# Kernel optimization log

Hardware: AMD Instinct MI355X
Metric: run time of the kernel (lower is better)

The kernel has to match this reference:

```python
import jax, jax.numpy as jnp
import numpy as np

E = 32      # feature/query dim
H = 4       # heads
HD = E // H # head dim = 8
N_LAYERS = 12
N_Q = 16
B = 128
S = 512


def _mha(q, kv, Wqkv, bqkv, Wo, bo):
    # PyTorch nn.MultiheadAttention (batch_first), eval mode (no dropout).
    Wq, Wk, Wv = jnp.split(Wqkv, 3, axis=0)   # each [E, E]
    bq, bk, bv = jnp.split(bqkv, 3)

    def heads(x, W, b):
        y = x @ W.T + b                         # [B, L, E]
        b_, l_, _ = y.shape
        return y.reshape(b_, l_, H, HD).transpose(0, 2, 1, 3)  # [B, H, L, HD]

    qh, kh, vh = heads(q, Wq, bq), heads(kv, Wk, bk), heads(kv, Wv, bv)
    scores = jnp.einsum('bhqd,bhkd->bhqk', qh, kh) / np.sqrt(HD).astype(np.float32)
    att = jax.nn.softmax(scores, axis=-1)
    o = jnp.einsum('bhqk,bhkd->bhqd', att, vh)
    o = o.transpose(0, 2, 1, 3).reshape(q.shape[0], q.shape[1], E)
    return o @ Wo.T + bo


def setup_inputs() -> dict:
    key = jax.random.key(0)
    ks = iter(jax.random.split(key, 64))
    g = lambda shape, s=0.05: (jax.random.normal(next(ks), shape, dtype=jnp.float32) * s)
    inp = {
        'x_omic': jax.random.normal(next(ks), (B, 80), dtype=jnp.float32),
        'x_path': jax.random.normal(next(ks), (B, S, E), dtype=jnp.float32),
        # frozen omic FFN encoder: 80 -> 64 -> 48 -> 32 -> 32, ELU each
        'omic_W0': g((64, 80)), 'omic_b0': g((64,)),
        'omic_W1': g((48, 64)), 'omic_b1': g((48,)),
        'omic_W2': g((32, 48)), 'omic_b2': g((32,)),
        'omic_W3': g((E, 32)),  'omic_b3': g((E,)),
        'ln_g': jnp.ones((E,), jnp.float32), 'ln_b': jnp.zeros((E,), jnp.float32),
        'corr_Wqkv': g((3 * E, E)), 'corr_bqkv': g((3 * E,)),
        'corr_Wo': g((E, E)), 'corr_bo': g((E,)),
        # 12 stacked query<->omic and query<->path cross-attentions
        'qo_Wqkv': g((N_LAYERS, 3 * E, E)), 'qo_bqkv': g((N_LAYERS, 3 * E)),
        'qo_Wo': g((N_LAYERS, E, E)), 'qo_bo': g((N_LAYERS, E)),
        'qp_Wqkv': g((N_LAYERS, 3 * E, E)), 'qp_bqkv': g((N_LAYERS, 3 * E)),
        'qp_Wo': g((N_LAYERS, E, E)), 'qp_bo': g((N_LAYERS, E)),
        # 12 stacked 2-layer FFNs (Linear-ReLU-Linear, no residual in source)
        'ffn_W1': g((N_LAYERS, E, E)), 'ffn_b1': g((N_LAYERS, E)),
        'ffn_W2': g((N_LAYERS, E, E)), 'ffn_b2': g((N_LAYERS, E)),
        'Qs': jax.random.normal(next(ks), (N_Q, E), dtype=jnp.float32),
        'grade_W': g((3, E)), 'grade_b': g((3,)),
        'haz_W': g((1, E)), 'haz_b': g((1,)),
    }
    return inp


def reference(x_omic, x_path, omic_W0, omic_b0, omic_W1, omic_b1, omic_W2, omic_b2,
              omic_W3, omic_b3, ln_g, ln_b, corr_Wqkv, corr_bqkv, corr_Wo, corr_bo,
              qo_Wqkv, qo_bqkv, qo_Wo, qo_bo, qp_Wqkv, qp_bqkv, qp_Wo, qp_bo,
              ffn_W1, ffn_b1, ffn_W2, ffn_b2, Qs, grade_W, grade_b, haz_W, haz_b):
    # frozen omic encoder (eval mode: AlphaDropout is identity)
    h = jax.nn.elu(x_omic @ omic_W0.T + omic_b0)
    h = jax.nn.elu(h @ omic_W1.T + omic_b1)
    h = jax.nn.elu(h @ omic_W2.T + omic_b2)
    omic_emb = jax.nn.elu(h @ omic_W3.T + omic_b3)[:, None, :]   # [B, 1, E]

    qs = jnp.broadcast_to(Qs[None], (x_omic.shape[0], N_Q, E))    # [B, 16, E]

    # correlation self-attention on LayerNorm(x_path), residual on raw x_path
    mu = jnp.mean(x_path, axis=-1, keepdims=True)
    var = jnp.var(x_path, axis=-1, keepdims=True)
    xn = (x_path - mu) / jnp.sqrt(var + 1e-5) * ln_g + ln_b
    img = x_path + _mha(xn, xn, corr_Wqkv, corr_bqkv, corr_Wo, corr_bo)

    for i in range(N_LAYERS):
        qs = _mha(qs, omic_emb, qo_Wqkv[i], qo_bqkv[i], qo_Wo[i], qo_bo[i])
        qs = _mha(qs, img, qp_Wqkv[i], qp_bqkv[i], qp_Wo[i], qp_bo[i])
        qs = jax.nn.relu(qs @ ffn_W1[i].T + ffn_b1[i]) @ ffn_W2[i].T + ffn_b2[i]

    features = qs.mean(axis=1)                                    # [B, E]
    grade = jax.nn.log_softmax(features @ grade_W.T + grade_b, axis=1)
    hazard = jax.nn.sigmoid(features @ haz_W.T + haz_b) * 6.0 - 3.0
    return features, grade, hazard
```

## Files before the change

kernel.cpp:

```cpp
#include <hip/hip_runtime.h>
#include <hip/hip_bf16.h>

typedef __attribute__((ext_vector_type(8))) short short8;
typedef __attribute__((ext_vector_type(4))) float f32x4;

__device__ __forceinline__ float elu1(float x) { return x > 0.f ? x : expm1f(x); }
__device__ __forceinline__ unsigned pkbf(float a, float b) {
  return (unsigned)__bfloat16_as_ushort(__float2bfloat16(a)) |
         ((unsigned)__bfloat16_as_ushort(__float2bfloat16(b)) << 16);
}
__device__ __forceinline__ unsigned pk_trunc(float a, float b) {
  return (__float_as_uint(a) >> 16) | (__float_as_uint(b) & 0xffff0000u);
}
__device__ __forceinline__ short8 cvt8(float4 a, float4 b, float s) {
  uint4 u = { pkbf(a.x * s, a.y * s), pkbf(a.z * s, a.w * s),
              pkbf(b.x * s, b.y * s), pkbf(b.z * s, b.w * s) };
  union { uint4 u4; short8 s8; } c; c.u4 = u; return c.s8;
}

__global__ __launch_bounds__(512, 4) void k_fattn(
    const float* __restrict__ xp, const float* __restrict__ ln_g, const float* __restrict__ ln_b,
    const float* __restrict__ Wqkv, const float* __restrict__ bqkv,
    ushort* __restrict__ obf)
{
  __shared__ ushort qlds[512 * 8];
  __shared__ ushort klds[512 * 8];
  __shared__ ushort vts[8 * 512];
  __shared__ ushort ps[8][2][16 * 64];

  const float sc = 0.35355339059327373f * 1.4426950408889634f;
  int tid = threadIdx.x, w = tid >> 6, lane = tid & 63;
  int g = lane >> 4, qr = lane & 15;
  int bh = blockIdx.x, b = bh >> 2, h = bh & 3;
  const short8 z8 = {0, 0, 0, 0, 0, 0, 0, 0};

  int wrow = (qr < 8) ? (h * 8 + qr) : (32 + h * 8 + qr - 8);
  float qsc = (qr < 8) ? sc : 1.f;
  const float4* wr = (const float4*)(Wqkv + wrow * 32 + g * 8);
  short8 wqk = cvt8(wr[0], wr[1], qsc);
  short8 wv = z8;
  if (qr < 8) {
    const float4* vr = (const float4*)(Wqkv + (64 + h * 8 + qr) * 32 + g * 8);
    wv = cvt8(vr[0], vr[1], 1.f);
  }
  f32x4 bqk, bv;
  #pragma unroll
  for (int r = 0; r < 4; ++r) {
    bqk[r] = (g < 2) ? bqkv[h * 8 + g * 4 + r] * sc : bqkv[32 + h * 8 + (g - 2) * 4 + r];
    bv[r]  = (g < 2) ? bqkv[64 + h * 8 + g * 4 + r] : 0.f;
  }
  const float4* lg4 = (const float4*)(ln_g + g * 8);
  const float4* lb4 = (const float4*)(ln_b + g * 8);
  float4 ga = lg4[0], gb2 = lg4[1], ba = lb4[0], bb2 = lb4[1];

  #pragma unroll
  for (int i = 0; i < 4; ++i) {
    int rloc = w * 64 + i * 16 + qr;
    const float4* xr = (const float4*)(xp + (b * 512 + rloc) * 32 + g * 8);
    float4 x0 = xr[0], x1 = xr[1];
    float s1 = x0.x + x0.y + x0.z + x0.w + x1.x + x1.y + x1.z + x1.w;
    float s2 = x0.x*x0.x + x0.y*x0.y + x0.z*x0.z + x0.w*x0.w
             + x1.x*x1.x + x1.y*x1.y + x1.z*x1.z + x1.w*x1.w;
    s1 += __shfl_xor(s1, 16); s1 += __shfl_xor(s1, 32);
    s2 += __shfl_xor(s2, 16); s2 += __shfl_xor(s2, 32);
    float mu = s1 * 0.03125f;
    float rs = rsqrtf(s2 * 0.03125f - mu * mu + 1e-5f);
    float4 n0 = { (x0.x-mu)*rs*ga.x+ba.x, (x0.y-mu)*rs*ga.y+ba.y,
                  (x0.z-mu)*rs*ga.z+ba.z, (x0.w-mu)*rs*ga.w+ba.w };
    float4 n1 = { (x1.x-mu)*rs*gb2.x+bb2.x, (x1.y-mu)*rs*gb2.y+bb2.y,
                  (x1.z-mu)*rs*gb2.z+bb2.z, (x1.w-mu)*rs*gb2.w+bb2.w };
    short8 bx = cvt8(n0, n1, 1.f);

    f32x4 cqk = __builtin_amdgcn_mfma_f32_16x16x32_bf16(wqk, bx, bqk, 0, 0, 0);
    f32x4 cv  = __builtin_amdgcn_mfma_f32_16x16x32_bf16(wv,  bx, bv,  0, 0, 0);
    uint2 o2 = { pkbf(cqk[0], cqk[1]), pkbf(cqk[2], cqk[3]) };
    ushort* dst = (g < 2) ? qlds : klds;
    *(uint2*)(dst + rloc * 8 + (g & 1) * 4) = o2;
    if (g < 2) {
      #pragma unroll
      for (int r = 0; r < 4; ++r)
        vts[(g * 4 + r) * 512 + rloc] = __bfloat16_as_ushort(__float2bfloat16(cv[r]));
    }
  }
  __syncthreads();

  const short8 one8 = {(short)0x3F80, (short)0x3F80, (short)0x3F80, (short)0x3F80,
                       (short)0x3F80, (short)0x3F80, (short)0x3F80, (short)0x3F80};
  unsigned swz = (unsigned)(qr & 7) << 4;
  char* p0 = (char*)&ps[w][0][0] + qr * 128;
  char* p1 = (char*)&ps[w][1][0] + qr * 128;

  #pragma unroll
  for (int p = 0; p < 2; ++p) {
    int qbase = w * 64 + p * 32;
    short8 qf0 = (g == 0) ? *(const short8*)(qlds + (qbase + qr) * 8) : z8;
    short8 qf1 = (g == 0) ? *(const short8*)(qlds + (qbase + 16 + qr) * 8) : z8;
    f32x4 ot0 = {0.f, 0.f, 0.f, 0.f}, ot1 = {0.f, 0.f, 0.f, 0.f};

    for (int c = 0; c < 8; ++c) {
      const short8* vp = (const short8*)(vts + qr * 512 + c * 64 + g * 8);
      short8 vf0 = (qr < 8) ? vp[0] : (qr == 8 ? one8 : z8);
      short8 vf1 = (qr < 8) ? vp[4] : (qr == 8 ? one8 : z8);
      #pragma unroll
      for (int t = 0; t < 4; ++t) {
        short8 af = (g == 0) ? *(const short8*)(klds + (c * 64 + t * 16 + qr) * 8) : z8;
        f32x4 sa = __builtin_amdgcn_mfma_f32_16x16x32_bf16(af, qf0, (f32x4){0.f,0.f,0.f,0.f}, 0, 0, 0);
        f32x4 sb = __builtin_amdgcn_mfma_f32_16x16x32_bf16(af, qf1, (f32x4){0.f,0.f,0.f,0.f}, 0, 0, 0);
        unsigned off = (unsigned)((t * 16 + g * 4) << 1) ^ swz;
        uint2 pa = { pk_trunc(__builtin_amdgcn_exp2f(sa[0]), __builtin_amdgcn_exp2f(sa[1])),
                     pk_trunc(__builtin_amdgcn_exp2f(sa[2]), __builtin_amdgcn_exp2f(sa[3])) };
        uint2 pb2 = { pk_trunc(__builtin_amdgcn_exp2f(sb[0]), __builtin_amdgcn_exp2f(sb[1])),
                      pk_trunc(__builtin_amdgcn_exp2f(sb[2]), __builtin_amdgcn_exp2f(sb[3])) };
        *(uint2*)(p0 + off) = pa;
        *(uint2*)(p1 + off) = pb2;
      }
      #pragma unroll
      for (int tp = 0; tp < 2; ++tp) {
        unsigned off = (unsigned)((tp * 32 + g * 8) << 1) ^ swz;
        short8 vv = tp ? vf1 : vf0;
        short8 pba = *(const short8*)(p0 + off);
        short8 pbb = *(const short8*)(p1 + off);
        ot0 = __builtin_amdgcn_mfma_f32_16x16x32_bf16(vv, pba, ot0, 0, 0, 0);
        ot1 = __builtin_amdgcn_mfma_f32_16x16x32_bf16(vv, pbb, ot1, 0, 0, 0);
      }
    }
    #pragma unroll
    for (int qg = 0; qg < 2; ++qg) {
      f32x4 ot = qg ? ot1 : ot0;
      float lpv = __shfl(ot[0], 32 + qr, 64);
      float rl = 1.f / lpv;
      if (g < 2) {
        int rowg = bh * 512 + qbase + qg * 16 + qr;
        uint2 o2 = { pkbf(ot[0] * rl, ot[1] * rl), pkbf(ot[2] * rl, ot[3] * rl) };
        *(uint2*)((unsigned*)obf + rowg * 4 + g * 2) = o2;
      }
    }
  }
}

__global__ __launch_bounds__(256) void k_final(
    const ushort* __restrict__ obf, const float* __restrict__ xp,
    const float* __restrict__ Wo, const float* __restrict__ bo,
    const float* __restrict__ xo,
    const float* __restrict__ oW0, const float* __restrict__ ob0,
    const float* __restrict__ oW1, const float* __restrict__ ob1,
    const float* __restrict__ oW2, const float* __restrict__ ob2,
    const float* __restrict__ oW3, const float* __restrict__ ob3,
    const float* __restrict__ qoW, const float* __restrict__ qob,
    const float* __restrict__ qoWo, const float* __restrict__ qobo,
    const float* __restrict__ qpW, const float* __restrict__ qpb,
    const float* __restrict__ qpWo, const float* __restrict__ qpbo,
    const float* __restrict__ fW1, const float* __restrict__ fb1,
    const float* __restrict__ fW2, const float* __restrict__ fb2,
    const float* __restrict__ gW, const float* __restrict__ gb,
    const float* __restrict__ hW, const float* __restrict__ hb,
    float* __restrict__ out)
{
  __shared__ float4 imgl[512 * 8];
  __shared__ float p[4][512];
  __shared__ float partial[8][4][32];
  __shared__ float buf1[80], buf2[64];
  __shared__ float emb[32], qbar[32], qh[32], u[4][32], cc4[4], lsum[4], ctx4[4][32], t32[32], o32[32];
  int b = blockIdx.x, tid = threadIdx.x;
  int w = tid >> 6, lane = tid & 63, g = lane >> 4, qr = lane & 15;

  {
    short8 wa[2]; f32x4 bc2[2];
    #pragma unroll
    for (int t = 0; t < 2; ++t) {
      const float4* wrr = (const float4*)(Wo + (t * 16 + qr) * 32 + g * 8);
      wa[t] = cvt8(wrr[0], wrr[1], 1.f);
      const float4 bb = *(const float4*)(bo + t * 16 + g * 4);
      bc2[t] = (f32x4){bb.x, bb.y, bb.z, bb.w};
    }
    #pragma unroll
    for (int j = 0; j < 8; ++j) {
      int rloc = j * 64 + w * 16 + qr;
      short8 ob = *(const short8*)(obf + ((b * 4 + g) * 512 + rloc) * 8);
      #pragma unroll
      for (int t = 0; t < 2; ++t) {
        f32x4 ct = __builtin_amdgcn_mfma_f32_16x16x32_bf16(wa[t], ob, bc2[t], 0, 0, 0);
        int e4 = t * 4 + g;
        float4 xv = *(const float4*)(xp + (b * 512 + rloc) * 32 + e4 * 4);
        imgl[rloc * 8 + (e4 ^ (rloc & 7))] =
            (float4){ xv.x + ct[0], xv.y + ct[1], xv.z + ct[2], xv.w + ct[3] };
      }
    }
  }
  __syncthreads();

  if (tid < 80) buf1[tid] = xo[b * 80 + tid];
  __syncthreads();
  if (tid < 64) { float a = ob0[tid]; const float* wgt = oW0 + tid * 80;
    for (int e = 0; e < 80; ++e) a += buf1[e] * wgt[e]; buf2[tid] = elu1(a); }
  __syncthreads();
  if (tid < 48) { float a = ob1[tid]; const float* wgt = oW1 + tid * 64;
    for (int e = 0; e < 64; ++e) a += buf2[e] * wgt[e]; buf1[tid] = elu1(a); }
  __syncthreads();
  if (tid < 32) { float a = ob2[tid]; const float* wgt = oW2 + tid * 48;
    for (int e = 0; e < 48; ++e) a += buf1[e] * wgt[e]; buf2[tid] = elu1(a); }
  __syncthreads();
  if (tid < 32) { float a = ob3[tid]; const float* wgt = oW3 + tid * 32;
    for (int e = 0; e < 32; ++e) a += buf2[e] * wgt[e]; emb[tid] = elu1(a); }
  __syncthreads();

  if (tid < 32) { float a = qob[64 + tid]; const float* wgt = qoW + (64 + tid) * 32;
    for (int e = 0; e < 32; ++e) a += emb[e] * wgt[e]; t32[tid] = a; }
  __syncthreads();
  if (tid < 32) { float a = qobo[tid]; const float* wgt = qoWo + tid * 32;
    for (int e = 0; e < 32; ++e) a += t32[e] * wgt[e]; qbar[tid] = a; }
  __syncthreads();

  if (tid < 32) { float a = qpb[tid]; const float* wgt = qpW + tid * 32;
    for (int e = 0; e < 32; ++e) a += qbar[e] * wgt[e]; qh[tid] = a; }
  __syncthreads();
  if (tid < 128) {
    int hh = tid >> 5, e = tid & 31;
    float a = 0.f;
    #pragma unroll
    for (int d = 0; d < 8; ++d) a += qh[hh * 8 + d] * qpW[(32 + hh * 8 + d) * 32 + e];
    u[hh][e] = a;
    if (e == 0) { float c2 = 0.f; for (int d = 0; d < 8; ++d) c2 += qh[hh * 8 + d] * qpb[32 + hh * 8 + d]; cc4[hh] = c2; }
  }
  __syncthreads();

  #pragma unroll
  for (int j = 0; j < 8; ++j) {
    int idx = tid + j * 256; int hh = idx >> 9, kk = idx & 511;
    const float* uh = u[hh];
    float a = cc4[hh];
    #pragma unroll
    for (int e4 = 0; e4 < 8; ++e4) {
      float4 t = imgl[kk * 8 + (e4 ^ (kk & 7))];
      a += uh[e4 * 4] * t.x + uh[e4 * 4 + 1] * t.y + uh[e4 * 4 + 2] * t.z + uh[e4 * 4 + 3] * t.w;
    }
    p[hh][kk] = __builtin_amdgcn_exp2f(fminf(a * 0.51006979f, 115.f));
  }
  __syncthreads();
  {
    int ww = tid >> 6, ln2 = tid & 63;
    float a = 0.f;
    for (int kk = ln2; kk < 512; kk += 64) a += p[ww][kk];
    #pragma unroll
    for (int m = 32; m >= 1; m >>= 1) a += __shfl_xor(a, m, 64);
    if (ln2 == 0) lsum[ww] = 1.f / a;
  }
  {
    int e = tid & 31, ch = tid >> 5;
    float a0 = 0.f, a1 = 0.f, a2 = 0.f, a3 = 0.f;
    for (int kk = ch * 64; kk < ch * 64 + 64; ++kk) {
      float val = ((const float*)&imgl[kk * 8 + ((e >> 2) ^ (kk & 7))])[e & 3];
      a0 += p[0][kk] * val; a1 += p[1][kk] * val; a2 += p[2][kk] * val; a3 += p[3][kk] * val;
    }
    partial[ch][0][e] = a0; partial[ch][1][e] = a1; partial[ch][2][e] = a2; partial[ch][3][e] = a3;
  }
  __syncthreads();
  if (tid < 128) {
    int hh = tid >> 5, e = tid & 31;
    float a = 0.f;
    #pragma unroll
    for (int ch = 0; ch < 8; ++ch) a += partial[ch][hh][e];
    ctx4[hh][e] = a * lsum[hh];
  }
  __syncthreads();
  if (tid < 32) { int hh = tid >> 3;
    float a = qpb[64 + tid]; const float* wgt = qpW + (64 + tid) * 32;
    for (int e = 0; e < 32; ++e) a += ctx4[hh][e] * wgt[e]; o32[tid] = a; }
  __syncthreads();
  if (tid < 32) { float a = qpbo[tid]; const float* wgt = qpWo + tid * 32;
    for (int e = 0; e < 32; ++e) a += o32[e] * wgt[e]; t32[tid] = a; }
  __syncthreads();

  if (tid < 32) { float a = fb1[tid]; const float* wgt = fW1 + tid * 32;
    for (int e = 0; e < 32; ++e) a += t32[e] * wgt[e]; o32[tid] = fmaxf(a, 0.f); }
  __syncthreads();
  if (tid < 32) { float a = fb2[tid]; const float* wgt = fW2 + tid * 32;
    for (int e = 0; e < 32; ++e) a += o32[e] * wgt[e]; qbar[tid] = a; }
  __syncthreads();

  if (tid < 32) out[b * 32 + tid] = qbar[tid];
  if (tid == 0) {
    float g0 = gb[0], g1 = gb[1], g2 = gb[2];
    for (int e = 0; e < 32; ++e) { float f = qbar[e]; g0 += f * gW[e]; g1 += f * gW[32 + e]; g2 += f * gW[64 + e]; }
    float m = fmaxf(g0, fmaxf(g1, g2));
    float lse = m + logf(expf(g0 - m) + expf(g1 - m) + expf(g2 - m));
    float* og = out + 4096;
    og[b * 3 + 0] = g0 - lse; og[b * 3 + 1] = g1 - lse; og[b * 3 + 2] = g2 - lse;
    float hz = hb[0];
    for (int e = 0; e < 32; ++e) hz += qbar[e] * hW[e];
    out[4480 + b] = 1.f / (1.f + expf(-hz)) * 6.f - 3.f;
  }
}

extern "C" void kernel_launch(void* const* d_in, const int* in_sizes, int n_in,
                              void* d_out, int out_size, void* d_ws, size_t ws_size,
                              hipStream_t stream) {
  const float* x_omic = (const float*)d_in[0];
  const float* x_path = (const float*)d_in[1];
  const float* oW0 = (const float*)d_in[2];  const float* ob0 = (const float*)d_in[3];
  const float* oW1 = (const float*)d_in[4];  const float* ob1 = (const float*)d_in[5];
  const float* oW2 = (const float*)d_in[6];  const float* ob2 = (const float*)d_in[7];
  const float* oW3 = (const float*)d_in[8];  const float* ob3 = (const float*)d_in[9];
  const float* ln_g = (const float*)d_in[10]; const float* ln_b = (const float*)d_in[11];
  const float* cW  = (const float*)d_in[12]; const float* cb  = (const float*)d_in[13];
  const float* cWo = (const float*)d_in[14]; const float* cbo = (const float*)d_in[15];
  const float* qoW = (const float*)d_in[16]; const float* qob = (const float*)d_in[17];
  const float* qoWo = (const float*)d_in[18]; const float* qobo = (const float*)d_in[19];
  const float* qpW = (const float*)d_in[20]; const float* qpb = (const float*)d_in[21];
  const float* qpWo = (const float*)d_in[22]; const float* qpbo = (const float*)d_in[23];
  const float* fW1 = (const float*)d_in[24]; const float* fb1 = (const float*)d_in[25];
  const float* fW2 = (const float*)d_in[26]; const float* fb2 = (const float*)d_in[27];
  const float* gW = (const float*)d_in[29]; const float* gb = (const float*)d_in[30];
  const float* hW = (const float*)d_in[31]; const float* hb = (const float*)d_in[32];

  float* out = (float*)d_out;
  ushort* obf = (ushort*)d_ws;

  const int L = 11;
  k_fattn<<<512, 512, 0, stream>>>(x_path, ln_g, ln_b, cW, cb, obf);
  k_final<<<128, 256, 0, stream>>>(obf, x_path, cWo, cbo, x_omic,
      oW0, ob0, oW1, ob1, oW2, ob2, oW3, ob3,
      qoW + L * 96 * 32, qob + L * 96, qoWo + L * 32 * 32, qobo + L * 32,
      qpW + L * 96 * 32, qpb + L * 96, qpWo + L * 32 * 32, qpbo + L * 32,
      fW1 + L * 32 * 32, fb1 + L * 32, fW2 + L * 32 * 32, fb2 + L * 32,
      gW, gb, hW, hb, out);
}
```

Measured before the change: 53.78 us.

## Restructure flash attention into one pass over four query tiles; widen final kernel

The attention kernel now loads all four 16-row Q fragments of a wave at once. It streams each K/V chunk a single time, running QK, exp and PV for every Q tile through one reused per-wave P buffer. This halves the LDS used for P and removes the redundant second pass over K/V. Packing exp values to bf16 now uses a single byte-permute instead of shift and mask. The K-operand masking and the zero V rows are dropped because they do not affect the output rows that are written. Separately, the final kernel doubles its block to 512 threads, splitting the image projection, score and context loops across more waves with more partial sums. The cost is higher register pressure from four accumulators and four Q fragments per wave.

```diff
diff --git a/kernel.cpp b/kernel.cpp
--- a/kernel.cpp
+++ b/kernel.cpp
@@ -9,13 +9,13 @@
   return (unsigned)__bfloat16_as_ushort(__float2bfloat16(a)) |
          ((unsigned)__bfloat16_as_ushort(__float2bfloat16(b)) << 16);
 }
-__device__ __forceinline__ unsigned pk_trunc(float a, float b) {
-  return (__float_as_uint(a) >> 16) | (__float_as_uint(b) & 0xffff0000u);
-}
 __device__ __forceinline__ short8 cvt8(float4 a, float4 b, float s) {
   uint4 u = { pkbf(a.x * s, a.y * s), pkbf(a.z * s, a.w * s),
               pkbf(b.x * s, b.y * s), pkbf(b.z * s, b.w * s) };
   union { uint4 u4; short8 s8; } c; c.u4 = u; return c.s8;
+}
+__device__ __forceinline__ unsigned pk_perm(float a, float b) {
+  return __builtin_amdgcn_perm(__float_as_uint(b), __float_as_uint(a), 0x07060302u);
 }
 
 __global__ __launch_bounds__(512, 4) void k_fattn(
@@ -26,7 +26,7 @@
   __shared__ ushort qlds[512 * 8];
   __shared__ ushort klds[512 * 8];
   __shared__ ushort vts[8 * 512];
-  __shared__ ushort ps[8][2][16 * 64];
+  __shared__ ushort ps[8][16 * 64];
 
   const float sc = 0.35355339059327373f * 1.4426950408889634f;
   int tid = threadIdx.x, w = tid >> 6, lane = tid & 63;
@@ -87,58 +87,63 @@
   const short8 one8 = {(short)0x3F80, (short)0x3F80, (short)0x3F80, (short)0x3F80,
                        (short)0x3F80, (short)0x3F80, (short)0x3F80, (short)0x3F80};
   unsigned swz = (unsigned)(qr & 7) << 4;
-  char* p0 = (char*)&ps[w][0][0] + qr * 128;
-  char* p1 = (char*)&ps[w][1][0] + qr * 128;
+  char* pw = (char*)&ps[w][0] + qr * 128;
+
+  int qbase = w * 64;
+  short8 qf0 = (g == 0) ? *(const short8*)(qlds + (qbase + qr) * 8) : z8;
+  short8 qf1 = (g == 0) ? *(const short8*)(qlds + (qbase + 16 + qr) * 8) : z8;
+  short8 qf2 = (g == 0) ? *(const short8*)(qlds + (qbase + 32 + qr) * 8) : z8;
+  short8 qf3 = (g == 0) ? *(const short8*)(qlds + (qbase + 48 + qr) * 8) : z8;
+  f32x4 ot0 = {0.f,0.f,0.f,0.f}, ot1 = {0.f,0.f,0.f,0.f};
+  f32x4 ot2 = {0.f,0.f,0.f,0.f}, ot3 = {0.f,0.f,0.f,0.f};
+
+#define QKPV(QF, OT) do {                                                       \
+    _Pragma("unroll")                                                           \
+    for (int t = 0; t < 4; ++t) {                                               \
+      short8 af = *(const short8*)(kbase + t * 128);    \
+      f32x4 s4 = __builtin_amdgcn_mfma_f32_16x16x32_bf16(af, QF,                \
+                   (f32x4){0.f,0.f,0.f,0.f}, 0, 0, 0);                          \
+      unsigned off = (unsigned)((t * 16 + g * 4) << 1) ^ swz;                   \
+      uint2 pk2 = { pk_perm(__builtin_amdgcn_exp2f(s4[0]),                      \
+                            __builtin_amdgcn_exp2f(s4[1])),                     \
+                    pk_perm(__builtin_amdgcn_exp2f(s4[2]),                      \
+                            __builtin_amdgcn_exp2f(s4[3])) };                   \
+      *(uint2*)(pw + off) = pk2;                                                \
+    }                                                                           \
+    {                                                                           \
+      short8 pb0 = *(const short8*)(pw + ((unsigned)((g * 8) << 1) ^ swz));     \
+      OT = __builtin_amdgcn_mfma_f32_16x16x32_bf16(vf0, pb0, OT, 0, 0, 0);      \
+      short8 pb1 = *(const short8*)(pw + ((unsigned)((32 + g * 8) << 1) ^ swz));\
+      OT = __builtin_amdgcn_mfma_f32_16x16x32_bf16(vf1, pb1, OT, 0, 0, 0);      \
+    }                                                                           \
+  } while (0)
+
+  for (int c = 0; c < 8; ++c) {
+    const short8* vp = (const short8*)(vts + qr * 512 + c * 64 + g * 8);
+    short8 vf0 = (qr < 8) ? vp[0] : one8;
+    short8 vf1 = (qr < 8) ? vp[4] : one8;
+    const ushort* kbase = klds + c * 64 * 8 + qr * 8;
+    QKPV(qf0, ot0);
+    QKPV(qf1, ot1);
+    QKPV(qf2, ot2);
+    QKPV(qf3, ot3);
+  }
+#undef QKPV
 
   #pragma unroll
-  for (int p = 0; p < 2; ++p) {
-    int qbase = w * 64 + p * 32;
-    short8 qf0 = (g == 0) ? *(const short8*)(qlds + (qbase + qr) * 8) : z8;
-    short8 qf1 = (g == 0) ? *(const short8*)(qlds + (qbase + 16 + qr) * 8) : z8;
-    f32x4 ot0 = {0.f, 0.f, 0.f, 0.f}, ot1 = {0.f, 0.f, 0.f, 0.f};
-
-    for (int c = 0; c < 8; ++c) {
-      const short8* vp = (const short8*)(vts + qr * 512 + c * 64 + g * 8);
-      short8 vf0 = (qr < 8) ? vp[0] : (qr == 8 ? one8 : z8);
-      short8 vf1 = (qr < 8) ? vp[4] : (qr == 8 ? one8 : z8);
-      #pragma unroll
-      for (int t = 0; t < 4; ++t) {
-        short8 af = (g == 0) ? *(const short8*)(klds + (c * 64 + t * 16 + qr) * 8) : z8;
-        f32x4 sa = __builtin_amdgcn_mfma_f32_16x16x32_bf16(af, qf0, (f32x4){0.f,0.f,0.f,0.f}, 0, 0, 0);
-        f32x4 sb = __builtin_amdgcn_mfma_f32_16x16x32_bf16(af, qf1, (f32x4){0.f,0.f,0.f,0.f}, 0, 0, 0);
-        unsigned off = (unsigned)((t * 16 + g * 4) << 1) ^ swz;
-        uint2 pa = { pk_trunc(__builtin_amdgcn_exp2f(sa[0]), __builtin_amdgcn_exp2f(sa[1])),
-                     pk_trunc(__builtin_amdgcn_exp2f(sa[2]), __builtin_amdgcn_exp2f(sa[3])) };
-        uint2 pb2 = { pk_trunc(__builtin_amdgcn_exp2f(sb[0]), __builtin_amdgcn_exp2f(sb[1])),
-                      pk_trunc(__builtin_amdgcn_exp2f(sb[2]), __builtin_amdgcn_exp2f(sb[3])) };
-        *(uint2*)(p0 + off) = pa;
-        *(uint2*)(p1 + off) = pb2;
-      }
-      #pragma unroll
-      for (int tp = 0; tp < 2; ++tp) {
-        unsigned off = (unsigned)((tp * 32 + g * 8) << 1) ^ swz;
-        short8 vv = tp ? vf1 : vf0;
-        short8 pba = *(const short8*)(p0 + off);
-        short8 pbb = *(const short8*)(p1 + off);
-        ot0 = __builtin_amdgcn_mfma_f32_16x16x32_bf16(vv, pba, ot0, 0, 0, 0);
-        ot1 = __builtin_amdgcn_mfma_f32_16x16x32_bf16(vv, pbb, ot1, 0, 0, 0);
-      }
-    }
-    #pragma unroll
-    for (int qg = 0; qg < 2; ++qg) {
-      f32x4 ot = qg ? ot1 : ot0;
-      float lpv = __shfl(ot[0], 32 + qr, 64);
-      float rl = 1.f / lpv;
-      if (g < 2) {
-        int rowg = bh * 512 + qbase + qg * 16 + qr;
-        uint2 o2 = { pkbf(ot[0] * rl, ot[1] * rl), pkbf(ot[2] * rl, ot[3] * rl) };
-        *(uint2*)((unsigned*)obf + rowg * 4 + g * 2) = o2;
-      }
-    }
-  }
-}
-
-__global__ __launch_bounds__(256) void k_final(
+  for (int i = 0; i < 4; ++i) {
+    f32x4 ot = (i == 0) ? ot0 : (i == 1) ? ot1 : (i == 2) ? ot2 : ot3;
+    float lpv = __shfl(ot[0], 32 + qr, 64);
+    float rl = 1.f / lpv;
+    if (g < 2) {
+      int rowg = bh * 512 + qbase + i * 16 + qr;
+      uint2 o2 = { pkbf(ot[0] * rl, ot[1] * rl), pkbf(ot[2] * rl, ot[3] * rl) };
+      *(uint2*)((unsigned*)obf + rowg * 4 + g * 2) = o2;
+    }
+  }
+}
+
+__global__ __launch_bounds__(512) void k_final(
     const ushort* __restrict__ obf, const float* __restrict__ xp,
     const float* __restrict__ Wo, const float* __restrict__ bo,
     const float* __restrict__ xo,
@@ -158,7 +163,7 @@
 {
   __shared__ float4 imgl[512 * 8];
   __shared__ float p[4][512];
-  __shared__ float partial[8][4][32];
+  __shared__ float partial[16][4][32];
   __shared__ float buf1[80], buf2[64];
   __shared__ float emb[32], qbar[32], qh[32], u[4][32], cc4[4], lsum[4], ctx4[4][32], t32[32], o32[32];
   int b = blockIdx.x, tid = threadIdx.x;
@@ -174,8 +179,8 @@
       bc2[t] = (f32x4){bb.x, bb.y, bb.z, bb.w};
     }
     #pragma unroll
-    for (int j = 0; j < 8; ++j) {
-      int rloc = j * 64 + w * 16 + qr;
+    for (int j = 0; j < 4; ++j) {
+      int rloc = j * 128 + w * 16 + qr;
       short8 ob = *(const short8*)(obf + ((b * 4 + g) * 512 + rloc) * 8);
       #pragma unroll
       for (int t = 0; t < 2; ++t) {
@@ -225,8 +230,8 @@
   __syncthreads();
 
   #pragma unroll
-  for (int j = 0; j < 8; ++j) {
-    int idx = tid + j * 256; int hh = idx >> 9, kk = idx & 511;
+  for (int j = 0; j < 4; ++j) {
+    int idx = tid + j * 512; int hh = idx >> 9, kk = idx & 511;
     const float* uh = u[hh];
     float a = cc4[hh];
     #pragma unroll
@@ -237,7 +242,7 @@
     p[hh][kk] = __builtin_amdgcn_exp2f(fminf(a * 0.51006979f, 115.f));
   }
   __syncthreads();
-  {
+  if (tid < 256) {
     int ww = tid >> 6, ln2 = tid & 63;
     float a = 0.f;
     for (int kk = ln2; kk < 512; kk += 64) a += p[ww][kk];
@@ -248,7 +253,7 @@
   {
     int e = tid & 31, ch = tid >> 5;
     float a0 = 0.f, a1 = 0.f, a2 = 0.f, a3 = 0.f;
-    for (int kk = ch * 64; kk < ch * 64 + 64; ++kk) {
+    for (int kk = ch * 32; kk < ch * 32 + 32; ++kk) {
       float val = ((const float*)&imgl[kk * 8 + ((e >> 2) ^ (kk & 7))])[e & 3];
       a0 += p[0][kk] * val; a1 += p[1][kk] * val; a2 += p[2][kk] * val; a3 += p[3][kk] * val;
     }
@@ -259,7 +264,7 @@
     int hh = tid >> 5, e = tid & 31;
     float a = 0.f;
     #pragma unroll
-    for (int ch = 0; ch < 8; ++ch) a += partial[ch][hh][e];
+    for (int ch = 0; ch < 16; ++ch) a += partial[ch][hh][e];
     ctx4[hh][e] = a * lsum[hh];
   }
   __syncthreads();
@@ -318,7 +323,7 @@
 
   const int L = 11;
   k_fattn<<<512, 512, 0, stream>>>(x_path, ln_g, ln_b, cW, cb, obf);
-  k_final<<<128, 256, 0, stream>>>(obf, x_path, cWo, cbo, x_omic,
+  k_final<<<128, 512, 0, stream>>>(obf, x_path, cWo, cbo, x_omic,
       oW0, ob0, oW1, ob1, oW2, ob2, oW3, ob3,
       qoW + L * 96 * 32, qob + L * 96, qoWo + L * 32 * 32, qobo + L * 32,
       qpW + L * 96 * 32, qpb + L * 96, qpWo + L * 32 * 32, qpbo + L * 32,
```

Result: faster. 49.77 us (-7.4%).
